# Kernel tuning notes

Hardware: AMD Instinct MI355X
Metric: run time of the kernel (lower is better)

The kernel has to match this reference:

```python
import jax, jax.numpy as jnp
import numpy as np


def dct_matrix(N, dtype=jnp.float32):
    # DCT-II orthonormal basis: D[k, n] = s_k * cos(pi * (n + 0.5) * k / N)
    n = jnp.arange(N, dtype=dtype)
    k = jnp.arange(N, dtype=dtype)
    M = jnp.cos(jnp.pi * (n[None, :] + 0.5) * k[:, None] / N)
    scale = jnp.full((N,), jnp.sqrt(2.0 / N), dtype=dtype).at[0].set(jnp.sqrt(1.0 / N))
    return scale[:, None] * M  # [K, N]


def setup_inputs() -> dict:
    key = jax.random.key(0)
    k1, k2, k3, k4 = jax.random.split(key, 4)
    B, C, H, W = 64, 3, 512, 512
    x = jax.random.normal(k1, (B, C, H, W), dtype=jnp.float32)
    attention = jax.random.uniform(k2, (H, W), dtype=jnp.float32)
    row_weights = jax.random.uniform(k3, (H,), dtype=jnp.float32)
    col_weights = jax.random.uniform(k4, (W,), dtype=jnp.float32)
    return {"x": x, "attention": attention, "row_weights": row_weights,
            "col_weights": col_weights}


def reference(x, attention, row_weights, col_weights):
    B, C, H, W = x.shape
    Dw = dct_matrix(W, x.dtype)  # DCT along last axis
    Dh = dct_matrix(H, x.dtype)  # DCT along second-to-last axis
    # dct(x, axis=-1): contract columns; dct(., axis=-2): contract rows
    x_dct = jnp.einsum('kh,bchw,lw->bckl', Dh, x, Dw)
    gray = x_dct.mean(axis=1)                 # [B, H, W]
    weighted = gray * attention               # [B, H, W]
    row_sum = weighted.mean(axis=2)           # [B, H]
    col_sum = weighted.mean(axis=1)           # [B, W]
    row_output = (row_sum * row_weights).mean(axis=1)  # [B]
    col_output = (col_sum * col_weights).mean(axis=1)  # [B]
    return jax.nn.sigmoid(jnp.stack([col_output, row_output], axis=1))  # [B, 2]
```

## Files before the change

kernel.cpp:

```cpp
#include <hip/hip_runtime.h>
#include <hip/hip_bf16.h>
#include <math.h>


typedef __attribute__((ext_vector_type(8))) short bf16x8;
typedef __attribute__((ext_vector_type(4))) float f32x4;

#define NFULL 512
#define HWTOT 262144
#define SCALE_M (1.0f / 786432.0f)

static __device__ __forceinline__ unsigned short f_to_bf16(float f) {
  union { float f; unsigned int i; } v; v.f = f;
  unsigned int r = v.i + 0x7FFFu + ((v.i >> 16) & 1u);
  return (unsigned short)(r >> 16);
}

__global__ void k0_prep(const float* __restrict__ att,
                        const float* __restrict__ cw,
                        unsigned short* __restrict__ DT,
                        unsigned short* __restrict__ Abf,
                        unsigned short* __restrict__ Acw) {
  int idx = blockIdx.x * blockDim.x + threadIdx.x;
  int n = idx >> 9;
  int k = idx & 511;
  unsigned int ph = ((unsigned int)(2 * n + 1) * (unsigned int)k) & 2047u;
  float s = (k == 0) ? 0.04419417382415922f
                     : 0.0625f;
  float c = s * cospif((float)ph * (1.0f / 1024.0f));
  DT[idx] = f_to_bf16(c);
  float a = att[idx];
  Abf[idx] = f_to_bf16(a);
  Acw[idx] = f_to_bf16(a * cw[k]);
}

__global__ void ka_gemm(const unsigned short* __restrict__ DT,
                        const unsigned short* __restrict__ Abf,
                        const unsigned short* __restrict__ Acw,
                        const float* __restrict__ rw,
                        unsigned short* __restrict__ GrowT,
                        unsigned short* __restrict__ GcT) {
  int wave = (blockIdx.x * blockDim.x + threadIdx.x) >> 6;
  int lane = threadIdx.x & 63;
  int tk = wave >> 5, tw = wave & 31;
  int row_a = tk * 16 + (lane & 15);
  int row_b = tw * 16 + (lane & 15);
  int koff = (lane >> 4) * 8;

  const bf16x8* Ap = (const bf16x8*)(Abf + row_a * NFULL);
  const bf16x8* Cp = (const bf16x8*)(Acw + row_a * NFULL);
  const bf16x8* Bp = (const bf16x8*)(DT  + row_b * NFULL);

  f32x4 accG = {0.f, 0.f, 0.f, 0.f};
  f32x4 accC = {0.f, 0.f, 0.f, 0.f};
#pragma unroll 4
  for (int l0 = 0; l0 < NFULL; l0 += 32) {
    int e = (l0 + koff) >> 3;
    bf16x8 a = Ap[e];
    bf16x8 c = Cp[e];
    bf16x8 b = Bp[e];
    accG = __builtin_amdgcn_mfma_f32_16x16x32_bf16(a, b, accG, 0, 0, 0);
    accC = __builtin_amdgcn_mfma_f32_16x16x32_bf16(c, b, accC, 0, 0, 0);
  }
  int col = lane & 15, r0 = (lane >> 4) * 4;
  int w  = tw * 16 + col;
  int k0 = tk * 16 + r0;
  unsigned int g0 = f_to_bf16(accG[0] * rw[k0 + 0]) | ((unsigned int)f_to_bf16(accG[1] * rw[k0 + 1]) << 16);
  unsigned int g1 = f_to_bf16(accG[2] * rw[k0 + 2]) | ((unsigned int)f_to_bf16(accG[3] * rw[k0 + 3]) << 16);
  unsigned int c0 = f_to_bf16(accC[0]) | ((unsigned int)f_to_bf16(accC[1]) << 16);
  unsigned int c1 = f_to_bf16(accC[2]) | ((unsigned int)f_to_bf16(accC[3]) << 16);
  uint2* pg = (uint2*)(GrowT + w * NFULL + k0);
  uint2* pc = (uint2*)(GcT   + w * NFULL + k0);
  *pg = make_uint2(g0, g1);
  *pc = make_uint2(c0, c1);
}

__global__ void kb_gemm(const unsigned short* __restrict__ DT,
                        const unsigned short* __restrict__ GrowT,
                        const unsigned short* __restrict__ GcT,
                        float* __restrict__ Mrow,
                        float* __restrict__ Mcol) {
  int wave = (blockIdx.x * blockDim.x + threadIdx.x) >> 6;
  int lane = threadIdx.x & 63;
  int th = wave >> 5, tw = wave & 31;
  int row_a = th * 16 + (lane & 15);
  int row_b = tw * 16 + (lane & 15);
  int koff = (lane >> 4) * 8;

  const bf16x8* Ap = (const bf16x8*)(DT    + row_a * NFULL);
  const bf16x8* Rp = (const bf16x8*)(GrowT + row_b * NFULL);
  const bf16x8* Cp = (const bf16x8*)(GcT   + row_b * NFULL);

  f32x4 accR = {0.f, 0.f, 0.f, 0.f};
  f32x4 accC = {0.f, 0.f, 0.f, 0.f};
#pragma unroll 4
  for (int k0 = 0; k0 < NFULL; k0 += 32) {
    int e = (k0 + koff) >> 3;
    bf16x8 a  = Ap[e];
    bf16x8 bR = Rp[e];
    bf16x8 bC = Cp[e];
    accR = __builtin_amdgcn_mfma_f32_16x16x32_bf16(a, bR, accR, 0, 0, 0);
    accC = __builtin_amdgcn_mfma_f32_16x16x32_bf16(a, bC, accC, 0, 0, 0);
  }
  int col = lane & 15, r0 = (lane >> 4) * 4;
  int h0 = th * 16 + r0;
  int w  = tw * 16 + col;
#pragma unroll
  for (int j = 0; j < 4; ++j) {
    Mrow[(h0 + j) * NFULL + w] = accR[j] * SCALE_M;
    Mcol[(h0 + j) * NFULL + w] = accC[j] * SCALE_M;
  }
}

#define NBLK 32
__global__ void kc_dot(const float* __restrict__ x,
                       const float* __restrict__ Mcol,
                       const float* __restrict__ Mrow,
                       float* __restrict__ partial) {
  int b   = blockIdx.x >> 5;
  int sub = blockIdx.x & 31;
  int tid = threadIdx.x;
  const float4* xb = (const float4*)x + (size_t)b * 196608;
  const float4* mc = (const float4*)Mcol;
  const float4* mr = (const float4*)Mrow;

  float a0 = 0.f, a1 = 0.f;
  int base = sub * 2048 + tid;
#pragma unroll
  for (int it = 0; it < 8; ++it) {
    int i = base + it * 256;
    float4 x0 = xb[i];
    float4 x1 = xb[i + 65536];
    float4 x2 = xb[i + 131072];
    float4 m0 = mc[i];
    float4 m1 = mr[i];
    float sx = x0.x + x1.x + x2.x;
    float sy = x0.y + x1.y + x2.y;
    float sz = x0.z + x1.z + x2.z;
    float sw = x0.w + x1.w + x2.w;
    a0 += sx * m0.x + sy * m0.y + sz * m0.z + sw * m0.w;
    a1 += sx * m1.x + sy * m1.y + sz * m1.z + sw * m1.w;
  }
  __shared__ float s0[256];
  __shared__ float s1[256];
  s0[tid] = a0; s1[tid] = a1;
  __syncthreads();
#pragma unroll
  for (int off = 128; off > 0; off >>= 1) {
    if (tid < off) { s0[tid] += s0[tid + off]; s1[tid] += s1[tid + off]; }
    __syncthreads();
  }
  if (tid == 0) {
    partial[(b * NBLK + sub) * 2 + 0] = s0[0];
    partial[(b * NBLK + sub) * 2 + 1] = s1[0];
  }
}

__global__ void kd_final(const float* __restrict__ partial, float* __restrict__ out) {
  int t = threadIdx.x;
  int b = t >> 1, o = t & 1;
  float s = 0.f;
#pragma unroll
  for (int j = 0; j < NBLK; ++j) s += partial[(b * NBLK + j) * 2 + o];
  out[b * 2 + o] = 1.0f / (1.0f + expf(-s));
}

extern "C" void kernel_launch(void* const* d_in, const int* in_sizes, int n_in,
                              void* d_out, int out_size, void* d_ws, size_t ws_size,
                              hipStream_t stream) {
  const float* x   = (const float*)d_in[0];
  const float* att = (const float*)d_in[1];
  const float* rw  = (const float*)d_in[2];
  const float* cw  = (const float*)d_in[3];
  float* out = (float*)d_out;

  unsigned short* DT    = (unsigned short*)d_ws;
  unsigned short* Abf   = DT    + HWTOT;
  unsigned short* Acw   = Abf   + HWTOT;
  unsigned short* GrowT = Acw   + HWTOT;
  unsigned short* GcT   = GrowT + HWTOT;
  float* Mrow    = (float*)(GcT + HWTOT);
  float* Mcol    = Mrow + HWTOT;
  float* partial = Mcol + HWTOT;

  k0_prep<<<1024, 256, 0, stream>>>(att, cw, DT, Abf, Acw);
  ka_gemm<<<256, 256, 0, stream>>>(DT, Abf, Acw, rw, GrowT, GcT);
  kb_gemm<<<256, 256, 0, stream>>>(DT, GrowT, GcT, Mrow, Mcol);
  kc_dot<<<64 * NBLK, 256, 0, stream>>>(x, Mcol, Mrow, partial);
  kd_final<<<1, 128, 0, stream>>>(partial, out);
}
```

Measured before the change: 59.11 us.

## Fuse the two DCT GEMMs into one kernel and fold the final reduction into the dot kernel

The two back-to-back GEMM kernels become one kernel. Each block keeps its 16-column intermediate in shared memory instead of writing it to global, and the row-weight scaling moves into the prep step. The dot kernel now reuses its M-matrix registers across 8 batches, loads x with nontemporal hints, reduces with wave shuffles, and finishes the sigmoid in the last block through an atomic counter, which removes the final kernel launch. The trade-off is that the fused GEMM runs on only 32 blocks, so the M computation has much less parallelism and could become a serial bottleneck.

```diff
diff --git a/kernel.cpp b/kernel.cpp
--- a/kernel.cpp
+++ b/kernel.cpp
@@ -9,6 +9,7 @@
 #define NFULL 512
 #define HWTOT 262144
 #define SCALE_M (1.0f / 786432.0f)
+#define KC_BLOCKS 512
 
 static __device__ __forceinline__ unsigned short f_to_bf16(float f) {
   union { float f; unsigned int i; } v; v.f = f;
@@ -17,152 +18,161 @@
 }
 
 __global__ void k0_prep(const float* __restrict__ att,
+                        const float* __restrict__ rw,
                         const float* __restrict__ cw,
                         unsigned short* __restrict__ DT,
-                        unsigned short* __restrict__ Abf,
-                        unsigned short* __restrict__ Acw) {
+                        unsigned short* __restrict__ Arw,
+                        unsigned short* __restrict__ Acw,
+                        int* __restrict__ counter) {
   int idx = blockIdx.x * blockDim.x + threadIdx.x;
-  int n = idx >> 9;
-  int k = idx & 511;
-  unsigned int ph = ((unsigned int)(2 * n + 1) * (unsigned int)k) & 2047u;
-  float s = (k == 0) ? 0.04419417382415922f
+  int r = idx >> 9;
+  int c = idx & 511;
+  unsigned int ph = ((unsigned int)(2 * r + 1) * (unsigned int)c) & 2047u;
+  float s = (c == 0) ? 0.04419417382415922f
                      : 0.0625f;
-  float c = s * cospif((float)ph * (1.0f / 1024.0f));
-  DT[idx] = f_to_bf16(c);
+  DT[idx] = f_to_bf16(s * cospif((float)ph * (1.0f / 1024.0f)));
   float a = att[idx];
-  Abf[idx] = f_to_bf16(a);
-  Acw[idx] = f_to_bf16(a * cw[k]);
+  Arw[idx] = f_to_bf16(a * rw[r]);
+  Acw[idx] = f_to_bf16(a * cw[c]);
+  if (idx == 0) *counter = 0;
 }
 
-__global__ void ka_gemm(const unsigned short* __restrict__ DT,
-                        const unsigned short* __restrict__ Abf,
-                        const unsigned short* __restrict__ Acw,
-                        const float* __restrict__ rw,
-                        unsigned short* __restrict__ GrowT,
-                        unsigned short* __restrict__ GcT) {
-  int wave = (blockIdx.x * blockDim.x + threadIdx.x) >> 6;
-  int lane = threadIdx.x & 63;
-  int tk = wave >> 5, tw = wave & 31;
-  int row_a = tk * 16 + (lane & 15);
-  int row_b = tw * 16 + (lane & 15);
-  int koff = (lane >> 4) * 8;
+__global__ __launch_bounds__(256) void kM(const unsigned short* __restrict__ DT,
+                                          const unsigned short* __restrict__ Arw,
+                                          const unsigned short* __restrict__ Acw,
+                                          float* __restrict__ Mrow,
+                                          float* __restrict__ Mcol) {
+  __shared__ unsigned short Tsh[2][16 * 520];
+  int w0 = blockIdx.x * 16;
+  int tid = threadIdx.x;
+  int lane = tid & 63, wv = tid >> 6;
+  int l16 = lane & 15;
+  int koff8 = (lane >> 4) * 8;
+  int r4 = (lane >> 4) * 4;
 
-  const bf16x8* Ap = (const bf16x8*)(Abf + row_a * NFULL);
-  const bf16x8* Cp = (const bf16x8*)(Acw + row_a * NFULL);
-  const bf16x8* Bp = (const bf16x8*)(DT  + row_b * NFULL);
+  const bf16x8* Bp = (const bf16x8*)(DT + (w0 + l16) * NFULL);
 
-  f32x4 accG = {0.f, 0.f, 0.f, 0.f};
-  f32x4 accC = {0.f, 0.f, 0.f, 0.f};
+  for (int t = 0; t < 8; ++t) {
+    int kt = wv * 8 + t;
+    const bf16x8* A1 = (const bf16x8*)(Arw + (kt * 16 + l16) * NFULL);
+    const bf16x8* A2 = (const bf16x8*)(Acw + (kt * 16 + l16) * NFULL);
+    f32x4 acc1 = {0.f, 0.f, 0.f, 0.f};
+    f32x4 acc2 = {0.f, 0.f, 0.f, 0.f};
 #pragma unroll 4
-  for (int l0 = 0; l0 < NFULL; l0 += 32) {
-    int e = (l0 + koff) >> 3;
-    bf16x8 a = Ap[e];
-    bf16x8 c = Cp[e];
-    bf16x8 b = Bp[e];
-    accG = __builtin_amdgcn_mfma_f32_16x16x32_bf16(a, b, accG, 0, 0, 0);
-    accC = __builtin_amdgcn_mfma_f32_16x16x32_bf16(c, b, accC, 0, 0, 0);
+    for (int l0 = 0; l0 < NFULL; l0 += 32) {
+      int e = (l0 + koff8) >> 3;
+      bf16x8 b = Bp[e];
+      acc1 = __builtin_amdgcn_mfma_f32_16x16x32_bf16(A1[e], b, acc1, 0, 0, 0);
+      acc2 = __builtin_amdgcn_mfma_f32_16x16x32_bf16(A2[e], b, acc2, 0, 0, 0);
+    }
+    int k0 = kt * 16 + r4;
+    unsigned int p10 = f_to_bf16(acc1[0]) | ((unsigned int)f_to_bf16(acc1[1]) << 16);
+    unsigned int p11 = f_to_bf16(acc1[2]) | ((unsigned int)f_to_bf16(acc1[3]) << 16);
+    unsigned int p20 = f_to_bf16(acc2[0]) | ((unsigned int)f_to_bf16(acc2[1]) << 16);
+    unsigned int p21 = f_to_bf16(acc2[2]) | ((unsigned int)f_to_bf16(acc2[3]) << 16);
+    *(uint2*)&Tsh[0][l16 * 520 + k0] = make_uint2(p10, p11);
+    *(uint2*)&Tsh[1][l16 * 520 + k0] = make_uint2(p20, p21);
   }
-  int col = lane & 15, r0 = (lane >> 4) * 4;
-  int w  = tw * 16 + col;
-  int k0 = tk * 16 + r0;
-  unsigned int g0 = f_to_bf16(accG[0] * rw[k0 + 0]) | ((unsigned int)f_to_bf16(accG[1] * rw[k0 + 1]) << 16);
-  unsigned int g1 = f_to_bf16(accG[2] * rw[k0 + 2]) | ((unsigned int)f_to_bf16(accG[3] * rw[k0 + 3]) << 16);
-  unsigned int c0 = f_to_bf16(accC[0]) | ((unsigned int)f_to_bf16(accC[1]) << 16);
-  unsigned int c1 = f_to_bf16(accC[2]) | ((unsigned int)f_to_bf16(accC[3]) << 16);
-  uint2* pg = (uint2*)(GrowT + w * NFULL + k0);
-  uint2* pc = (uint2*)(GcT   + w * NFULL + k0);
-  *pg = make_uint2(g0, g1);
-  *pc = make_uint2(c0, c1);
-}
+  __syncthreads();
 
-__global__ void kb_gemm(const unsigned short* __restrict__ DT,
-                        const unsigned short* __restrict__ GrowT,
-                        const unsigned short* __restrict__ GcT,
-                        float* __restrict__ Mrow,
-                        float* __restrict__ Mcol) {
-  int wave = (blockIdx.x * blockDim.x + threadIdx.x) >> 6;
-  int lane = threadIdx.x & 63;
-  int th = wave >> 5, tw = wave & 31;
-  int row_a = th * 16 + (lane & 15);
-  int row_b = tw * 16 + (lane & 15);
-  int koff = (lane >> 4) * 8;
-
-  const bf16x8* Ap = (const bf16x8*)(DT    + row_a * NFULL);
-  const bf16x8* Rp = (const bf16x8*)(GrowT + row_b * NFULL);
-  const bf16x8* Cp = (const bf16x8*)(GcT   + row_b * NFULL);
-
-  f32x4 accR = {0.f, 0.f, 0.f, 0.f};
-  f32x4 accC = {0.f, 0.f, 0.f, 0.f};
+  for (int t = 0; t < 8; ++t) {
+    int ht = wv * 8 + t;
+    const bf16x8* Ap = (const bf16x8*)(DT + (ht * 16 + l16) * NFULL);
+    f32x4 aR = {0.f, 0.f, 0.f, 0.f};
+    f32x4 aC = {0.f, 0.f, 0.f, 0.f};
 #pragma unroll 4
-  for (int k0 = 0; k0 < NFULL; k0 += 32) {
-    int e = (k0 + koff) >> 3;
-    bf16x8 a  = Ap[e];
-    bf16x8 bR = Rp[e];
-    bf16x8 bC = Cp[e];
-    accR = __builtin_amdgcn_mfma_f32_16x16x32_bf16(a, bR, accR, 0, 0, 0);
-    accC = __builtin_amdgcn_mfma_f32_16x16x32_bf16(a, bC, accC, 0, 0, 0);
-  }
-  int col = lane & 15, r0 = (lane >> 4) * 4;
-  int h0 = th * 16 + r0;
-  int w  = tw * 16 + col;
+    for (int k0s = 0; k0s < NFULL; k0s += 32) {
+      int e = (k0s + koff8) >> 3;
+      bf16x8 a = Ap[e];
+      bf16x8 b1 = *(const bf16x8*)&Tsh[0][l16 * 520 + k0s + koff8];
+      bf16x8 b2 = *(const bf16x8*)&Tsh[1][l16 * 520 + k0s + koff8];
+      aR = __builtin_amdgcn_mfma_f32_16x16x32_bf16(a, b1, aR, 0, 0, 0);
+      aC = __builtin_amdgcn_mfma_f32_16x16x32_bf16(a, b2, aC, 0, 0, 0);
+    }
+    int h0 = ht * 16 + r4, w = w0 + l16;
 #pragma unroll
-  for (int j = 0; j < 4; ++j) {
-    Mrow[(h0 + j) * NFULL + w] = accR[j] * SCALE_M;
-    Mcol[(h0 + j) * NFULL + w] = accC[j] * SCALE_M;
+    for (int j = 0; j < 4; ++j) {
+      Mrow[(h0 + j) * NFULL + w] = aR[j] * SCALE_M;
+      Mcol[(h0 + j) * NFULL + w] = aC[j] * SCALE_M;
+    }
   }
 }
 
-#define NBLK 32
-__global__ void kc_dot(const float* __restrict__ x,
-                       const float* __restrict__ Mcol,
-                       const float* __restrict__ Mrow,
-                       float* __restrict__ partial) {
-  int b   = blockIdx.x >> 5;
-  int sub = blockIdx.x & 31;
+__global__ __launch_bounds__(256) void kc_dot(const float* __restrict__ x,
+                                              const float* __restrict__ Mcol,
+                                              const float* __restrict__ Mrow,
+                                              float* __restrict__ partial,
+                                              int* __restrict__ counter,
+                                              float* __restrict__ out) {
+  int sub = blockIdx.x & 63;
+  int bg  = blockIdx.x >> 6;
   int tid = threadIdx.x;
-  const float4* xb = (const float4*)x + (size_t)b * 196608;
-  const float4* mc = (const float4*)Mcol;
-  const float4* mr = (const float4*)Mrow;
+  int base = sub * 1024 + tid;
 
-  float a0 = 0.f, a1 = 0.f;
-  int base = sub * 2048 + tid;
+  const f32x4* mc = (const f32x4*)Mcol;
+  const f32x4* mr = (const f32x4*)Mrow;
+  f32x4 mcr[4], mrr[4];
 #pragma unroll
-  for (int it = 0; it < 8; ++it) {
-    int i = base + it * 256;
-    float4 x0 = xb[i];
-    float4 x1 = xb[i + 65536];
-    float4 x2 = xb[i + 131072];
-    float4 m0 = mc[i];
-    float4 m1 = mr[i];
-    float sx = x0.x + x1.x + x2.x;
-    float sy = x0.y + x1.y + x2.y;
-    float sz = x0.z + x1.z + x2.z;
-    float sw = x0.w + x1.w + x2.w;
-    a0 += sx * m0.x + sy * m0.y + sz * m0.z + sw * m0.w;
-    a1 += sx * m1.x + sy * m1.y + sz * m1.z + sw * m1.w;
+  for (int it = 0; it < 4; ++it) {
+    mcr[it] = mc[base + it * 256];
+    mrr[it] = mr[base + it * 256];
   }
-  __shared__ float s0[256];
-  __shared__ float s1[256];
-  s0[tid] = a0; s1[tid] = a1;
+
+  float a0[8], a1[8];
+#pragma unroll
+  for (int q = 0; q < 8; ++q) { a0[q] = 0.f; a1[q] = 0.f; }
+
+#pragma unroll
+  for (int q = 0; q < 8; ++q) {
+    const f32x4* xb = (const f32x4*)x + (size_t)(bg * 8 + q) * 196608;
+    float s0 = 0.f, s1 = 0.f;
+#pragma unroll
+    for (int it = 0; it < 4; ++it) {
+      int i = base + it * 256;
+      f32x4 x0 = __builtin_nontemporal_load(xb + i);
+      f32x4 x1 = __builtin_nontemporal_load(xb + i + 65536);
+      f32x4 x2 = __builtin_nontemporal_load(xb + i + 131072);
+      f32x4 sv = x0 + x1 + x2;
+      f32x4 m0 = mcr[it], m1 = mrr[it];
+      s0 += sv.x * m0.x + sv.y * m0.y + sv.z * m0.z + sv.w * m0.w;
+      s1 += sv.x * m1.x + sv.y * m1.y + sv.z * m1.z + sv.w * m1.w;
+    }
+    a0[q] = s0; a1[q] = s1;
+  }
+
+  int lane = tid & 63, wv = tid >> 6;
+  __shared__ float red[4][16];
+#pragma unroll
+  for (int q = 0; q < 8; ++q) {
+    float v0 = a0[q], v1 = a1[q];
+#pragma unroll
+    for (int off = 32; off > 0; off >>= 1) {
+      v0 += __shfl_down(v0, off);
+      v1 += __shfl_down(v1, off);
+    }
+    if (lane == 0) { red[wv][q * 2] = v0; red[wv][q * 2 + 1] = v1; }
+  }
   __syncthreads();
-#pragma unroll
-  for (int off = 128; off > 0; off >>= 1) {
-    if (tid < off) { s0[tid] += s0[tid + off]; s1[tid] += s1[tid + off]; }
-    __syncthreads();
+  if (tid < 16) {
+    float s = red[0][tid] + red[1][tid] + red[2][tid] + red[3][tid];
+    int q = tid >> 1, o = tid & 1;
+    int b = bg * 8 + q;
+    partial[(b * 64 + sub) * 2 + o] = s;
   }
-  if (tid == 0) {
-    partial[(b * NBLK + sub) * 2 + 0] = s0[0];
-    partial[(b * NBLK + sub) * 2 + 1] = s1[0];
+  __threadfence();
+  __syncthreads();
+  __shared__ int lastf;
+  if (tid == 0) lastf = (atomicAdd(counter, 1) == KC_BLOCKS - 1);
+  __syncthreads();
+  if (lastf) {
+    __threadfence();
+    if (tid < 128) {
+      int b = tid >> 1, o = tid & 1;
+      float s = 0.f;
+      for (int sb = 0; sb < 64; ++sb) s += partial[(b * 64 + sb) * 2 + o];
+      out[b * 2 + o] = 1.0f / (1.0f + expf(-s));
+    }
   }
-}
-
-__global__ void kd_final(const float* __restrict__ partial, float* __restrict__ out) {
-  int t = threadIdx.x;
-  int b = t >> 1, o = t & 1;
-  float s = 0.f;
-#pragma unroll
-  for (int j = 0; j < NBLK; ++j) s += partial[(b * NBLK + j) * 2 + o];
-  out[b * 2 + o] = 1.0f / (1.0f + expf(-s));
 }
 
 extern "C" void kernel_launch(void* const* d_in, const int* in_sizes, int n_in,
@@ -174,18 +184,15 @@
   const float* cw  = (const float*)d_in[3];
   float* out = (float*)d_out;
 
-  unsigned short* DT    = (unsigned short*)d_ws;
-  unsigned short* Abf   = DT    + HWTOT;
-  unsigned short* Acw   = Abf   + HWTOT;
-  unsigned short* GrowT = Acw   + HWTOT;
-  unsigned short* GcT   = GrowT + HWTOT;
-  float* Mrow    = (float*)(GcT + HWTOT);
+  unsigned short* DT  = (unsigned short*)d_ws;
+  unsigned short* Arw = DT + HWTOT;
+  unsigned short* Acw = Arw + HWTOT;
+  float* Mrow    = (float*)(Acw + HWTOT);
   float* Mcol    = Mrow + HWTOT;
   float* partial = Mcol + HWTOT;
+  int*   counter = (int*)(partial + 8192);
 
-  k0_prep<<<1024, 256, 0, stream>>>(att, cw, DT, Abf, Acw);
-  ka_gemm<<<256, 256, 0, stream>>>(DT, Abf, Acw, rw, GrowT, GcT);
-  kb_gemm<<<256, 256, 0, stream>>>(DT, GrowT, GcT, Mrow, Mcol);
-  kc_dot<<<64 * NBLK, 256, 0, stream>>>(x, Mcol, Mrow, partial);
-  kd_final<<<1, 128, 0, stream>>>(partial, out);
+  k0_prep<<<1024, 256, 0, stream>>>(att, rw, cw, DT, Arw, Acw, counter);
+  kM<<<32, 256, 0, stream>>>(DT, Arw, Acw, Mrow, Mcol);
+  kc_dot<<<KC_BLOCKS, 256, 0, stream>>>(x, Mcol, Mrow, partial, counter, out);
 }
```

Result: slower. 169.0 us (+185.9%).
